# Kernel optimization log

Hardware: AMD Instinct MI355X
Metric: run time of the kernel (lower is better)

## Reference

```python
import jax, jax.numpy as jnp
import numpy as np

N, C, H, W = 4, 256, 64, 64
E = C // 2  # embed_dim = max(C//2, 1)


def setup_inputs() -> dict:
    key = jax.random.key(0)
    k1, k2, k3, k4 = jax.random.split(key, 4)
    x = jax.random.normal(k1, (N, C, H, W), dtype=jnp.float32)
    # 1x1 conv weights == channel-mixing matrices (bias=False), std=0.01 init
    W_theta = jax.random.normal(k2, (E, C), dtype=jnp.float32) * 0.01
    W_phi = jax.random.normal(k3, (E, C), dtype=jnp.float32) * 0.01
    W_proj = jax.random.normal(k4, (C, C), dtype=jnp.float32) * 0.01  # zero_init=False
    return {"x": x, "W_theta": W_theta, "W_phi": W_phi, "W_proj": W_proj}


def reference(x, W_theta, W_phi, W_proj):
    n, c, h, w = x.shape
    s = h * w
    xf = x.reshape(n, c, s)                      # [N, C, S]
    theta = jnp.einsum('ec,ncs->nes', W_theta, xf)  # [N, E, S]
    phi = jnp.einsum('ec,ncs->nes', W_phi, xf)      # [N, E, S]
    # f = theta^T @ phi, scaled by sqrt(embed_dim) (theta.shape[-1] after permute)
    scale = jnp.sqrt(jnp.asarray(theta.shape[1], dtype=x.dtype))
    f = jnp.einsum('nes,net->nst', theta, phi) / scale  # [N, S, S]
    f = jax.nn.softmax(f, axis=-1)
    # y = f @ g^T with g = x (unembedded values)
    y = jnp.einsum('nst,nct->ncs', f, xf)        # [N, C, S]
    residual = jnp.einsum('oc,ncs->nos', W_proj, y).reshape(n, c, h, w)
    return x + residual
```

## Files before the change

### kernel.cpp

```cpp
#include <hip/hip_runtime.h>
#include <cmath>

#define C_DIM 256
#define E_DIM 128
#define S_DIM 4096

typedef __bf16 bf16x8 __attribute__((ext_vector_type(8)));
typedef float  f32x4  __attribute__((ext_vector_type(4)));
typedef short  s16x8  __attribute__((ext_vector_type(8)));
typedef short  s16x4  __attribute__((ext_vector_type(4)));

__device__ __forceinline__ unsigned short f2bf(float f) {
  union { float f; unsigned u; } v; v.f = f;
  unsigned r = v.u + 0x7FFFu + ((v.u >> 16) & 1u);
  return (unsigned short)(r >> 16);
}
__device__ __forceinline__ unsigned short f2bf_tr(float f) {
  union { float f; unsigned u; } v; v.f = f;
  return (unsigned short)(v.u >> 16);
}
__device__ __forceinline__ bf16x8 as_bf(s16x8 v) {
  union { s16x8 s; bf16x8 b; } u; u.s = v; return u.b;
}

__global__ __launch_bounds__(256) void cast_w_kernel(
    const float* __restrict__ Wth, const float* __restrict__ Wph,
    const float* __restrict__ Wpr, short* __restrict__ Wb) {
  int t = blockIdx.x * 256 + threadIdx.x;
  int i = t * 4;
  const float* src; int j;
  if (i < 32768)      { src = Wth; j = i; }
  else if (i < 65536) { src = Wph; j = i - 32768; }
  else                { src = Wpr; j = i - 65536; }
  float4 v = *(const float4*)(src + j);
  s16x4 o;
  o[0] = (short)f2bf(v.x); o[1] = (short)f2bf(v.y);
  o[2] = (short)f2bf(v.z); o[3] = (short)f2bf(v.w);
  *(s16x4*)(Wb + i) = o;
}

__global__ __launch_bounds__(256) void mix_kernel(
    const float* __restrict__ x, const short* __restrict__ Wb,
    short* __restrict__ Qg, short* __restrict__ Kg, short* __restrict__ Xb,
    float qscale) {
  __shared__ short lxT[32 * C_DIM];
  int bid = blockIdx.x;
  int n = bid >> 7, s0 = (bid & 127) * 32;
  int tid = threadIdx.x;
  int wid = tid >> 6, lane = tid & 63, l15 = lane & 15, l4 = lane >> 4;

  {
    int cp = tid >> 1, su = tid & 1;
    const float* r0 = x + ((size_t)n * C_DIM + 2 * cp) * S_DIM + s0 + su * 16;
    const float* r1 = r0 + S_DIM;
    float a0[16], a1[16];
    #pragma unroll
    for (int j = 0; j < 4; ++j) {
      *(float4*)(a0 + 4 * j) = *(const float4*)(r0 + 4 * j);
      *(float4*)(a1 + 4 * j) = *(const float4*)(r1 + 4 * j);
    }
    short b0[16], b1[16];
    #pragma unroll
    for (int j = 0; j < 16; ++j) { b0[j] = (short)f2bf(a0[j]); b1[j] = (short)f2bf(a1[j]); }
    short* xb0 = Xb + ((size_t)n * C_DIM + 2 * cp) * S_DIM + s0 + su * 16;
    *(s16x8*)(xb0)             = *(s16x8*)(b0);
    *(s16x8*)(xb0 + 8)         = *(s16x8*)(b0 + 8);
    *(s16x8*)(xb0 + S_DIM)     = *(s16x8*)(b1);
    *(s16x8*)(xb0 + S_DIM + 8) = *(s16x8*)(b1 + 8);
    #pragma unroll
    for (int j = 0; j < 16; ++j) {
      int s = su * 16 + j;
      unsigned d = (unsigned)(unsigned short)b0[j] |
                   ((unsigned)(unsigned short)b1[j] << 16);
      *(unsigned*)((char*)lxT + s * 512 + ((4 * cp) ^ ((s & 7) << 4))) = d;
    }
  }
  __syncthreads();

  const short* Wq = Wb;
  const short* Wk = Wb + 32768;
  const f32x4 fzero = {0.f, 0.f, 0.f, 0.f};
  f32x4 accQ[2][2], accK[2][2];
  #pragma unroll
  for (int a = 0; a < 2; ++a)
    #pragma unroll
    for (int b = 0; b < 2; ++b) { accQ[a][b] = fzero; accK[a][b] = fzero; }

  #pragma unroll 2
  for (int kk = 0; kk < 8; ++kk) {
    bf16x8 bfr[2];
    #pragma unroll
    for (int nf = 0; nf < 2; ++nf) {
      int s = nf * 16 + l15;
      bfr[nf] = *(const bf16x8*)((char*)lxT + s * 512 +
                                 ((kk * 64 + l4 * 16) ^ ((s & 7) << 4)));
    }
    #pragma unroll
    for (int mf = 0; mf < 2; ++mf) {
      int e = wid * 32 + mf * 16 + l15;
      bf16x8 aq = *(const bf16x8*)(Wq + e * C_DIM + kk * 32 + l4 * 8);
      bf16x8 ak = *(const bf16x8*)(Wk + e * C_DIM + kk * 32 + l4 * 8);
      #pragma unroll
      for (int nf = 0; nf < 2; ++nf) {
        accQ[mf][nf] = __builtin_amdgcn_mfma_f32_16x16x32_bf16(aq, bfr[nf], accQ[mf][nf], 0, 0, 0);
        accK[mf][nf] = __builtin_amdgcn_mfma_f32_16x16x32_bf16(ak, bfr[nf], accK[mf][nf], 0, 0, 0);
      }
    }
  }

  #pragma unroll
  for (int mf = 0; mf < 2; ++mf) {
    #pragma unroll
    for (int nf = 0; nf < 2; ++nf) {
      int e = wid * 32 + mf * 16 + l4 * 4;
      int s = s0 + nf * 16 + l15;
      s16x4 pq, pk;
      #pragma unroll
      for (int r = 0; r < 4; ++r) {
        pq[r] = (short)f2bf(accQ[mf][nf][r] * qscale);
        pk[r] = (short)f2bf(accK[mf][nf][r]);
      }
      *(s16x4*)(Qg + ((size_t)n * S_DIM + s) * E_DIM + e) = pq;
      *(s16x4*)(Kg + ((size_t)n * S_DIM + s) * E_DIM + e) = pk;
    }
  }
}

__global__ __launch_bounds__(512, 2) void attn_kernel(
    const short* __restrict__ Qg, const short* __restrict__ Kg,
    const short* __restrict__ Xb, short* __restrict__ Yg) {
  __shared__ short lK[2 * 64 * E_DIM];
  __shared__ short lP[2 * 64 * 64];
  __shared__ float lsred[4 * 64];

  int bid = blockIdx.x;
  int xcd = bid & 7;
  int n   = xcd >> 1;
  int s0  = (((xcd & 1) << 5) + (bid >> 3)) * 64;

  int tid = threadIdx.x;
  int wid = tid >> 6, lane = tid & 63;
  int l15 = lane & 15, l4 = lane >> 4;

  const short* Kb = Kg + (size_t)n * S_DIM * E_DIM;
  const short* Vb = Xb + (size_t)n * (size_t)C_DIM * S_DIM;

  const f32x4 fzero = {0.f, 0.f, 0.f, 0.f};

  bf16x8 qf[4][4];
  float lsum[4];
  f32x4 acc[4][4];
  s16x8 kpre[4];
  s16x8 vpre[8];

  int tq = wid;
  int cq = wid - 4;
  int idx = tid & 255;
  int kr = idx >> 4, kc = idx & 15;

  if (wid < 4) {
    #pragma unroll
    for (int qs = 0; qs < 4; ++qs) {
      const short* qp = Qg + ((size_t)n * S_DIM + s0 + qs * 16 + l15) * E_DIM + l4 * 8;
      #pragma unroll
      for (int ec = 0; ec < 4; ++ec) qf[qs][ec] = *(const bf16x8*)(qp + ec * 32);
    }
    #pragma unroll
    for (int j = 0; j < 4; ++j) lsum[j] = 0.f;
  } else {
    #pragma unroll
    for (int a = 0; a < 4; ++a)
      #pragma unroll
      for (int b = 0; b < 4; ++b) acc[a][b] = fzero;
    s16x8 k0[4];
    #pragma unroll
    for (int j = 0; j < 4; ++j)
      k0[j] = *(const s16x8*)(Kb + (size_t)(kr + 16 * j) * E_DIM + kc * 8);
    #pragma unroll
    for (int j = 0; j < 4; ++j) {
      int r = kr + 16 * j;
      *(s16x8*)((char*)lK + r * 256 + ((kc * 16) ^ ((r & 7) << 4))) = k0[j];
    }
    #pragma unroll
    for (int j = 0; j < 4; ++j)
      kpre[j] = *(const s16x8*)(Kb + (size_t)(64 + kr + 16 * j) * E_DIM + kc * 8);
    #pragma unroll
    for (int kk = 0; kk < 2; ++kk)
      #pragma unroll
      for (int ct = 0; ct < 4; ++ct)
        vpre[kk * 4 + ct] = *(const s16x8*)(
            Vb + (size_t)(cq * 64 + ct * 16 + l15) * S_DIM + kk * 32 + l4 * 8);
  }
  __syncthreads();

  for (int i = 0; i <= 64; ++i) {
    if (wid < 4) {
      if (i < 64) {
        const char* kb = (const char*)lK + (i & 1) * 16384;
        f32x4 sc[4] = {fzero, fzero, fzero, fzero};
        int trow = tq * 16 + l15;
        int swz = (trow & 7) << 4;
        #pragma unroll
        for (int ec = 0; ec < 4; ++ec) {
          bf16x8 kf = *(const bf16x8*)(kb + trow * 256 + ((ec * 64 + l4 * 16) ^ swz));
          #pragma unroll
          for (int qs = 0; qs < 4; ++qs)
            sc[qs] = __builtin_amdgcn_mfma_f32_16x16x32_bf16(kf, qf[qs][ec], sc[qs], 0, 0, 0);
        }
        char* pw = (char*)lP + (i & 1) * 8192;
        int tb2 = tq * 32 + l4 * 8;
        #pragma unroll
        for (int qs = 0; qs < 4; ++qs) {
          float p0 = __builtin_amdgcn_exp2f(sc[qs][0]);
          float p1 = __builtin_amdgcn_exp2f(sc[qs][1]);
          float p2 = __builtin_amdgcn_exp2f(sc[qs][2]);
          float p3 = __builtin_amdgcn_exp2f(sc[qs][3]);
          lsum[qs] += (p0 + p1) + (p2 + p3);
          uint2 dd;
          dd.x = (unsigned)f2bf_tr(p0) | ((unsigned)f2bf_tr(p1) << 16);
          dd.y = (unsigned)f2bf_tr(p2) | ((unsigned)f2bf_tr(p3) << 16);
          int q = qs * 16 + l15;
          *(uint2*)(pw + q * 128 + (tb2 ^ ((q & 7) << 4))) = dd;
        }
      }
    } else {
      if (i <= 62) {
        char* kw = (char*)lK + ((i + 1) & 1) * 16384;
        #pragma unroll
        for (int j = 0; j < 4; ++j) {
          int r = kr + 16 * j;
          *(s16x8*)(kw + r * 256 + ((kc * 16) ^ ((r & 7) << 4))) = kpre[j];
        }
      }
      if (i >= 1) {
        const char* pr = (const char*)lP + ((i & 1) ^ 1) * 8192;
        #pragma unroll
        for (int kk = 0; kk < 2; ++kk) {
          bf16x8 pf[4];
          #pragma unroll
          for (int qs = 0; qs < 4; ++qs) {
            int q = qs * 16 + l15;
            pf[qs] = *(const bf16x8*)(pr + q * 128 + ((kk * 64 + l4 * 16) ^ ((q & 7) << 4)));
          }
          #pragma unroll
          for (int ct = 0; ct < 4; ++ct) {
            bf16x8 vf = as_bf(vpre[kk * 4 + ct]);
            #pragma unroll
            for (int qs = 0; qs < 4; ++qs)
              acc[qs][ct] = __builtin_amdgcn_mfma_f32_16x16x32_bf16(pf[qs], vf, acc[qs][ct], 0, 0, 0);
          }
        }
        if (i < 64) {
          #pragma unroll
          for (int kk = 0; kk < 2; ++kk)
            #pragma unroll
            for (int ct = 0; ct < 4; ++ct)
              vpre[kk * 4 + ct] = *(const s16x8*)(
                  Vb + (size_t)(cq * 64 + ct * 16 + l15) * S_DIM + i * 64 + kk * 32 + l4 * 8);
        }
      }
      if (i <= 61) {
        #pragma unroll
        for (int j = 0; j < 4; ++j)
          kpre[j] = *(const s16x8*)(Kb + (size_t)((i + 2) * 64 + kr + 16 * j) * E_DIM + kc * 8);
      }
    }
    asm volatile("s_waitcnt lgkmcnt(0)" ::: "memory");
    __builtin_amdgcn_s_barrier();
  }

  if (wid < 4) {
    #pragma unroll
    for (int qs = 0; qs < 4; ++qs) {
      float v = lsum[qs];
      v += __shfl_xor(v, 16);
      v += __shfl_xor(v, 32);
      if (lane < 16) lsred[tq * 64 + qs * 16 + l15] = v;
    }
  }
  __syncthreads();

  short* yst = lK;
  if (wid >= 4) {
    #pragma unroll
    for (int qs = 0; qs < 4; ++qs) {
      #pragma unroll
      for (int r = 0; r < 4; ++r) {
        int q = qs * 16 + l4 * 4 + r;
        float tot = lsred[q] + lsred[64 + q] + lsred[128 + q] + lsred[192 + q];
        float rl = 1.0f / tot;
        #pragma unroll
        for (int ct = 0; ct < 4; ++ct) {
          int c = cq * 64 + ct * 16 + l15;
          *(unsigned short*)((char*)yst + q * 512 + ((c * 2) ^ ((q & 7) << 4))) =
              f2bf_tr(acc[qs][ct][r] * rl);
        }
      }
    }
  }
  __syncthreads();

  int rr = tid >> 3, chb = tid & 7;
  #pragma unroll
  for (int it = 0; it < 4; ++it) {
    int ch = chb + 8 * it;
    s16x8 v = *(const s16x8*)((char*)yst + rr * 512 + ((ch * 16) ^ ((rr & 7) << 4)));
    *(s16x8*)(Yg + ((size_t)n * S_DIM + s0 + rr) * C_DIM + ch * 8) = v;
  }
}

__global__ __launch_bounds__(256) void proj_kernel(
    const short* __restrict__ Yg, const short* __restrict__ Wpb,
    const float* __restrict__ x, float* __restrict__ out) {
  int bid = blockIdx.x;
  int n = bid >> 7, s0 = (bid & 127) * 32;
  int tid = threadIdx.x;
  int wid = tid >> 6, lane = tid & 63, l15 = lane & 15, l4 = lane >> 4;

  const f32x4 fzero = {0.f, 0.f, 0.f, 0.f};
  f32x4 acc[2][4];
  #pragma unroll
  for (int a = 0; a < 2; ++a)
    #pragma unroll
    for (int b = 0; b < 4; ++b) acc[a][b] = fzero;

  const short* ybase = Yg + (size_t)n * S_DIM * C_DIM;

  #pragma unroll 2
  for (int kk = 0; kk < 8; ++kk) {
    bf16x8 af[2];
    #pragma unroll
    for (int mf = 0; mf < 2; ++mf)
      af[mf] = *(const bf16x8*)(ybase + (size_t)(s0 + mf * 16 + l15) * C_DIM +
                                kk * 32 + l4 * 8);
    #pragma unroll
    for (int nf = 0; nf < 4; ++nf) {
      int o = wid * 64 + nf * 16 + l15;
      bf16x8 bfr = *(const bf16x8*)(Wpb + o * C_DIM + kk * 32 + l4 * 8);
      #pragma unroll
      for (int mf = 0; mf < 2; ++mf)
        acc[mf][nf] = __builtin_amdgcn_mfma_f32_16x16x32_bf16(af[mf], bfr, acc[mf][nf], 0, 0, 0);
    }
  }

  #pragma unroll
  for (int mf = 0; mf < 2; ++mf) {
    #pragma unroll
    for (int nf = 0; nf < 4; ++nf) {
      int o = wid * 64 + nf * 16 + l15;
      size_t idx = ((size_t)n * C_DIM + o) * (size_t)S_DIM + s0 + mf * 16 + l4 * 4;
      float4 xv = *(const float4*)(x + idx);
      float4 r;
      r.x = xv.x + acc[mf][nf][0];
      r.y = xv.y + acc[mf][nf][1];
      r.z = xv.z + acc[mf][nf][2];
      r.w = xv.w + acc[mf][nf][3];
      *(float4*)(out + idx) = r;
    }
  }
}

extern "C" void kernel_launch(void* const* d_in, const int* in_sizes, int n_in,
                              void* d_out, int out_size, void* d_ws, size_t ws_size,
                              hipStream_t stream) {
  const float* x   = (const float*)d_in[0];
  const float* Wth = (const float*)d_in[1];
  const float* Wph = (const float*)d_in[2];
  const float* Wpr = (const float*)d_in[3];
  float* out = (float*)d_out;

  short* q_ws  = (short*)d_ws;
  short* k_ws  = q_ws  + (size_t)4 * S_DIM * E_DIM;
  short* xb_ws = k_ws  + (size_t)4 * S_DIM * E_DIM;
  short* y_ws  = xb_ws + (size_t)4 * C_DIM * S_DIM;
  short* wb_ws = y_ws  + (size_t)4 * S_DIM * C_DIM;

  float qscale = 1.4426950408889634f / sqrtf(128.0f);

  cast_w_kernel<<<128, 256, 0, stream>>>(Wth, Wph, Wpr, wb_ws);
  mix_kernel<<<512, 256, 0, stream>>>(x, wb_ws, q_ws, k_ws, xb_ws, qscale);
  attn_kernel<<<256, 512, 0, stream>>>(q_ws, k_ws, xb_ws, y_ws);
  proj_kernel<<<512, 256, 0, stream>>>(y_ws, wb_ws + 65536, x, out);
}
```

Before: 118.5 us.

## Unroll attention loop by two with ping-pong prefetch registers and MFMA priority

Unrolls the producer/consumer attention loop by two so LDS buffer indices are compile-time constants. K and V prefetches now go into separate even/odd register sets, and V loads are issued before the P·V MFMAs rather than after them. s_setprio raises wave priority around the MFMA blocks. The aim is to hide global-load latency and cut index arithmetic, at the cost of more live VGPRs, which could cause spills at the 512x2 launch bounds.

Result: slower. 207.1 us (+74.8%).

```diff
diff --git a/kernel.cpp b/kernel.cpp
--- a/kernel.cpp
+++ b/kernel.cpp
@@ -126,6 +126,89 @@
   }
 }
 
+
+#define QKT_BODY(KBUF)                                                        \
+  {                                                                           \
+    const char* kb = (const char*)lK + (KBUF) * 16384;                        \
+    char* pw = (char*)lP + (KBUF) * 8192;                                     \
+    f32x4 sc[4] = {fzero, fzero, fzero, fzero};                               \
+    int trow = tq * 16 + l15;                                                 \
+    int swz = (trow & 7) << 4;                                                \
+    __builtin_amdgcn_s_setprio(1);                                            \
+    _Pragma("unroll")                                                         \
+    for (int ec = 0; ec < 4; ++ec) {                                          \
+      bf16x8 kf = *(const bf16x8*)(kb + trow * 256 + ((ec * 64 + l4 * 16) ^ swz)); \
+      _Pragma("unroll")                                                       \
+      for (int qs = 0; qs < 4; ++qs)                                          \
+        sc[qs] = __builtin_amdgcn_mfma_f32_16x16x32_bf16(kf, qf[qs][ec], sc[qs], 0, 0, 0); \
+    }                                                                         \
+    __builtin_amdgcn_s_setprio(0);                                            \
+    int tb2 = tq * 32 + l4 * 8;                                               \
+    _Pragma("unroll")                                                         \
+    for (int qs = 0; qs < 4; ++qs) {                                          \
+      float p0 = __builtin_amdgcn_exp2f(sc[qs][0]);                           \
+      float p1 = __builtin_amdgcn_exp2f(sc[qs][1]);                           \
+      float p2 = __builtin_amdgcn_exp2f(sc[qs][2]);                           \
+      float p3 = __builtin_amdgcn_exp2f(sc[qs][3]);                           \
+      lsum[qs] += (p0 + p1) + (p2 + p3);                                      \
+      uint2 dd;                                                               \
+      dd.x = (unsigned)f2bf_tr(p0) | ((unsigned)f2bf_tr(p1) << 16);           \
+      dd.y = (unsigned)f2bf_tr(p2) | ((unsigned)f2bf_tr(p3) << 16);           \
+      int q = qs * 16 + l15;                                                  \
+      *(uint2*)(pw + q * 128 + (tb2 ^ ((q & 7) << 4))) = dd;                  \
+    }                                                                         \
+  }
+
+#define PV_VISSUE(vdst, TI)                                                   \
+  _Pragma("unroll")                                                           \
+  for (int kk = 0; kk < 2; ++kk)                                              \
+    _Pragma("unroll")                                                         \
+    for (int ct = 0; ct < 4; ++ct)                                            \
+      vdst[kk * 4 + ct] = *(const s16x8*)(                                    \
+          Vb + (size_t)(cq * 64 + ct * 16 + l15) * S_DIM + (TI) * 64 + kk * 32 + l4 * 8);
+
+#define PV_KCOMMIT(ksrc, KBUFW)                                               \
+  {                                                                           \
+    char* kw = (char*)lK + (KBUFW) * 16384;                                   \
+    _Pragma("unroll")                                                         \
+    for (int jj = 0; jj < 4; ++jj) {                                          \
+      int r = kr + 16 * jj;                                                   \
+      *(s16x8*)(kw + r * 256 + ((kc * 16) ^ ((r & 7) << 4))) = ksrc[jj];      \
+    }                                                                         \
+  }
+
+#define PV_KLOAD(kdst, TI)                                                    \
+  _Pragma("unroll")                                                           \
+  for (int jj = 0; jj < 4; ++jj)                                              \
+    kdst[jj] = *(const s16x8*)(Kb + (size_t)((TI) * 64 + kr + 16 * jj) * E_DIM + kc * 8);
+
+#define PV_MFMA(vsrc, PBUF)                                                   \
+  {                                                                           \
+    const char* pr = (const char*)lP + (PBUF) * 8192;                         \
+    _Pragma("unroll")                                                         \
+    for (int kk = 0; kk < 2; ++kk) {                                          \
+      bf16x8 pf[4];                                                           \
+      _Pragma("unroll")                                                       \
+      for (int qs = 0; qs < 4; ++qs) {                                        \
+        int q = qs * 16 + l15;                                                \
+        pf[qs] = *(const bf16x8*)(pr + q * 128 + ((kk * 64 + l4 * 16) ^ ((q & 7) << 4))); \
+      }                                                                       \
+      __builtin_amdgcn_s_setprio(1);                                          \
+      _Pragma("unroll")                                                       \
+      for (int ct = 0; ct < 4; ++ct) {                                        \
+        bf16x8 vf = as_bf(vsrc[kk * 4 + ct]);                                 \
+        _Pragma("unroll")                                                     \
+        for (int qs = 0; qs < 4; ++qs)                                        \
+          acc[qs][ct] = __builtin_amdgcn_mfma_f32_16x16x32_bf16(pf[qs], vf, acc[qs][ct], 0, 0, 0); \
+      }                                                                       \
+      __builtin_amdgcn_s_setprio(0);                                          \
+    }                                                                         \
+  }
+
+#define RAW_BARRIER()                                                         \
+  asm volatile("s_waitcnt lgkmcnt(0)" ::: "memory");                          \
+  __builtin_amdgcn_s_barrier();
+
 __global__ __launch_bounds__(512, 2) void attn_kernel(
     const short* __restrict__ Qg, const short* __restrict__ Kg,
     const short* __restrict__ Xb, short* __restrict__ Yg) {
@@ -150,8 +233,8 @@
   bf16x8 qf[4][4];
   float lsum[4];
   f32x4 acc[4][4];
-  s16x8 kpre[4];
-  s16x8 vpre[8];
+  s16x8 kpreE[4], kpreO[4];
+  s16x8 vpreE[8], vpreO[8];
 
   int tq = wid;
   int cq = wid - 4;
@@ -181,92 +264,34 @@
       int r = kr + 16 * j;
       *(s16x8*)((char*)lK + r * 256 + ((kc * 16) ^ ((r & 7) << 4))) = k0[j];
     }
-    #pragma unroll
-    for (int j = 0; j < 4; ++j)
-      kpre[j] = *(const s16x8*)(Kb + (size_t)(64 + kr + 16 * j) * E_DIM + kc * 8);
-    #pragma unroll
-    for (int kk = 0; kk < 2; ++kk)
-      #pragma unroll
-      for (int ct = 0; ct < 4; ++ct)
-        vpre[kk * 4 + ct] = *(const s16x8*)(
-            Vb + (size_t)(cq * 64 + ct * 16 + l15) * S_DIM + kk * 32 + l4 * 8);
-  }
-  __syncthreads();
-
-  for (int i = 0; i <= 64; ++i) {
+    PV_KLOAD(kpreO, 1);
+    PV_VISSUE(vpreE, 0);
+  }
+  RAW_BARRIER();
+
+  for (int j = 0; j < 32; ++j) {
+    int i0 = 2 * j;
     if (wid < 4) {
-      if (i < 64) {
-        const char* kb = (const char*)lK + (i & 1) * 16384;
-        f32x4 sc[4] = {fzero, fzero, fzero, fzero};
-        int trow = tq * 16 + l15;
-        int swz = (trow & 7) << 4;
-        #pragma unroll
-        for (int ec = 0; ec < 4; ++ec) {
-          bf16x8 kf = *(const bf16x8*)(kb + trow * 256 + ((ec * 64 + l4 * 16) ^ swz));
-          #pragma unroll
-          for (int qs = 0; qs < 4; ++qs)
-            sc[qs] = __builtin_amdgcn_mfma_f32_16x16x32_bf16(kf, qf[qs][ec], sc[qs], 0, 0, 0);
-        }
-        char* pw = (char*)lP + (i & 1) * 8192;
-        int tb2 = tq * 32 + l4 * 8;
-        #pragma unroll
-        for (int qs = 0; qs < 4; ++qs) {
-          float p0 = __builtin_amdgcn_exp2f(sc[qs][0]);
-          float p1 = __builtin_amdgcn_exp2f(sc[qs][1]);
-          float p2 = __builtin_amdgcn_exp2f(sc[qs][2]);
-          float p3 = __builtin_amdgcn_exp2f(sc[qs][3]);
-          lsum[qs] += (p0 + p1) + (p2 + p3);
-          uint2 dd;
-          dd.x = (unsigned)f2bf_tr(p0) | ((unsigned)f2bf_tr(p1) << 16);
-          dd.y = (unsigned)f2bf_tr(p2) | ((unsigned)f2bf_tr(p3) << 16);
-          int q = qs * 16 + l15;
-          *(uint2*)(pw + q * 128 + (tb2 ^ ((q & 7) << 4))) = dd;
-        }
-      }
+      QKT_BODY(0);
     } else {
-      if (i <= 62) {
-        char* kw = (char*)lK + ((i + 1) & 1) * 16384;
-        #pragma unroll
-        for (int j = 0; j < 4; ++j) {
-          int r = kr + 16 * j;
-          *(s16x8*)(kw + r * 256 + ((kc * 16) ^ ((r & 7) << 4))) = kpre[j];
-        }
-      }
-      if (i >= 1) {
-        const char* pr = (const char*)lP + ((i & 1) ^ 1) * 8192;
-        #pragma unroll
-        for (int kk = 0; kk < 2; ++kk) {
-          bf16x8 pf[4];
-          #pragma unroll
-          for (int qs = 0; qs < 4; ++qs) {
-            int q = qs * 16 + l15;
-            pf[qs] = *(const bf16x8*)(pr + q * 128 + ((kk * 64 + l4 * 16) ^ ((q & 7) << 4)));
-          }
-          #pragma unroll
-          for (int ct = 0; ct < 4; ++ct) {
-            bf16x8 vf = as_bf(vpre[kk * 4 + ct]);
-            #pragma unroll
-            for (int qs = 0; qs < 4; ++qs)
-              acc[qs][ct] = __builtin_amdgcn_mfma_f32_16x16x32_bf16(pf[qs], vf, acc[qs][ct], 0, 0, 0);
-          }
-        }
-        if (i < 64) {
-          #pragma unroll
-          for (int kk = 0; kk < 2; ++kk)
-            #pragma unroll
-            for (int ct = 0; ct < 4; ++ct)
-              vpre[kk * 4 + ct] = *(const s16x8*)(
-                  Vb + (size_t)(cq * 64 + ct * 16 + l15) * S_DIM + i * 64 + kk * 32 + l4 * 8);
-        }
-      }
-      if (i <= 61) {
-        #pragma unroll
-        for (int j = 0; j < 4; ++j)
-          kpre[j] = *(const s16x8*)(Kb + (size_t)((i + 2) * 64 + kr + 16 * j) * E_DIM + kc * 8);
-      }
-    }
-    asm volatile("s_waitcnt lgkmcnt(0)" ::: "memory");
-    __builtin_amdgcn_s_barrier();
+      if (j > 0)  PV_VISSUE(vpreE, i0);
+      PV_KCOMMIT(kpreO, 1);
+      if (j > 0)  PV_MFMA(vpreO, 1);
+      if (j < 31) PV_KLOAD(kpreE, i0 + 2);
+    }
+    RAW_BARRIER();
+    if (wid < 4) {
+      QKT_BODY(1);
+    } else {
+      PV_VISSUE(vpreO, i0 + 1);
+      if (j < 31) PV_KCOMMIT(kpreE, 0);
+      PV_MFMA(vpreE, 0);
+      if (j < 31) PV_KLOAD(kpreO, i0 + 3);
+    }
+    RAW_BARRIER();
+  }
+  if (wid >= 4) {
+    PV_MFMA(vpreO, 1);
   }
 
   if (wid < 4) {
```
